# Kernel optimization log

Hardware: AMD Instinct MI355X
Metric: run time of the kernel (lower is better)

The kernel has to match this reference:

```python
import jax, jax.numpy as jnp
import numpy as np

B, N, C = 8, 4096, 768
H, HD = 12, 64          # num_heads, head_dim = C // H
M = HD * 2              # rand_feat_dim
LAM = 0.3
NUM_STEP = 5


def setup_inputs() -> dict:
    key = jax.random.key(0)
    k1, k2, k3, k4 = jax.random.split(key, 4)
    x = jax.random.normal(k1, (B, N, C), dtype=jnp.float32)
    Wqkv = jax.random.normal(k2, (C, 2 * C), dtype=jnp.float32) * 0.02
    Wproj = jax.random.normal(k3, (C, C), dtype=jnp.float32) * 0.02
    bproj = jnp.zeros((C,), dtype=jnp.float32)
    rand_matrix = jax.random.normal(k4, (H, HD, M), dtype=jnp.float32)
    return {"x": x, "Wqkv": Wqkv, "Wproj": Wproj, "bproj": bproj,
            "rand_matrix": rand_matrix}


def _soft(z, t):
    # sign(z) * relu(|z| - t): soft-thresholding (ISTA proximal step)
    return jnp.sign(z) * jax.nn.relu(jnp.abs(z) - t)


def reference(x, Wqkv, Wproj, bproj, rand_matrix):
    Bn, Nn, Cn = x.shape
    Hh, hd, m = rand_matrix.shape
    scale = hd ** (-0.5)

    qkv = x @ Wqkv                                   # [B,N,2C]
    q = qkv[..., :Cn].reshape(Bn, Nn, Hh, hd).transpose(0, 2, 1, 3)  # [B,H,N,hd]
    v = qkv[..., Cn:].reshape(Bn, Nn, Hh, hd).transpose(0, 2, 1, 3)  # [B,H,N,hd]

    # random-feature map: exp(q @ proj - ||q||^2 / 2) / sqrt(m)
    qs = q * scale ** 0.5
    rf = jnp.exp(jnp.einsum('bhnd,hdm->bhnm', qs, rand_matrix)
                 - 0.5 * jnp.sum(qs * qs, axis=-1, keepdims=True)) / m ** 0.5
    # F.normalize(p=2, dim=-2): normalize over the sequence axis
    qn = rf / jnp.maximum(jnp.linalg.norm(rf, axis=-2, keepdims=True), 1e-12)

    kk = jnp.einsum('bhnm,bhnp->bhmp', qn, qn)       # [B,H,m,m]
    kv = jnp.einsum('bhnm,bhnd->bhmd', qn, v)        # [B,H,m,hd]

    # Lipschitz bound: max row L1 norm of kk, detached
    L = jax.lax.stop_gradient(
        jnp.max(jnp.sum(jnp.abs(kk), axis=-1), axis=-1))[..., None, None] + 1.0

    # unrolled ISTA soft-thresholding loop
    s = _soft(kv, LAM)
    for _ in range(NUM_STEP):
        s = _soft(s - (kk @ s - kv) / L, LAM / L)

    out = jnp.einsum('bhnm,bhmd->bhnd', qn, s)       # [B,H,N,hd]
    out = out.transpose(0, 2, 1, 3).reshape(Bn, Nn, Cn)
    return out @ Wproj + bproj
```

## Files before the change

### kernel.cpp

```cpp
#include <hip/hip_runtime.h>


typedef __attribute__((ext_vector_type(8))) short bf16x8;
typedef __attribute__((ext_vector_type(4))) float f32x4;

#define GLD16(gptr, lptr)                                                              \
  __builtin_amdgcn_global_load_lds((const __attribute__((address_space(1))) void*)(gptr), \
                                   (__attribute__((address_space(3))) void*)(lptr), 16, 0, 0)

__device__ __forceinline__ unsigned short f2bf(float f) {
  union { float f; unsigned int u; } v; v.f = f;
  unsigned int r = v.u + 0x7fffu + ((v.u >> 16) & 1u);
  return (unsigned short)(r >> 16);
}
__device__ __forceinline__ float bf2f(unsigned short s) {
  union { unsigned int u; float f; } v; v.u = ((unsigned int)s) << 16;
  return v.f;
}
__device__ __forceinline__ float rn_of(float css) {
  return 1.f / fmaxf(sqrtf(css), 1e-12f);
}

template<int ITERS>
__device__ __forceinline__ void gemm256_core(
    const unsigned short* __restrict__ A,
    const unsigned short* __restrict__ B,
    int ldk,
    f32x4 (&acc)[8][4],
    unsigned short* smem) {
  const int tid = threadIdx.x;
  const int lane = tid & 63, wave = tid >> 6;
  const int l16 = lane & 15, quad = lane >> 4;
  const int wr = wave >> 2, wc = wave & 3;
  const int rsw = l16 & 7;

#pragma unroll
  for (int i = 0; i < 8; i++)
#pragma unroll
    for (int j = 0; j < 4; j++)
#pragma unroll
      for (int r = 0; r < 4; r++) acc[i][j][r] = 0.f;

  const int srow0 = tid >> 3, sc0 = ((tid & 7) ^ (srow0 & 7)) << 3;
  const int srow1 = (tid + 512) >> 3, sc1 = ((tid & 7) ^ (srow1 & 7)) << 3;
  const int dstw = wave * 512;

  auto stageA = [&](int T, int h) {
    const unsigned short* g = A + (long)(h * 128) * ldk + T * 64;
    unsigned short* d = smem + (T & 1) * 32768 + h * 8192 + dstw;
    GLD16(g + (long)srow0 * ldk + sc0, d);
    GLD16(g + (long)srow1 * ldk + sc1, d + 4096);
  };
  auto stageB = [&](int T, int h) {
    const unsigned short* g = B + (long)(h * 128) * ldk + T * 64;
    unsigned short* d = smem + (T & 1) * 32768 + 16384 + h * 8192 + dstw;
    GLD16(g + (long)srow0 * ldk + sc0, d);
    GLD16(g + (long)srow1 * ldk + sc1, d + 4096);
  };

  bf16x8 af[4][2], bn[4][2];

  auto rdA_ks = [&](int b, int mh, int ks) {
    const unsigned short* p = smem + b * 32768 + wr * 8192 + (mh * 64 + l16) * 64;
#pragma unroll
    for (int ii = 0; ii < 4; ii++)
      af[ii][ks] = *(const bf16x8*)(p + ii * 1024 + (((ks * 4 + quad) ^ rsw) << 3));
  };
  auto rdB_ks = [&](int b, int ks) {
    const unsigned short* p = smem + b * 32768 + 16384 + (wc >> 1) * 8192 +
                              ((wc & 1) * 64 + l16) * 64;
#pragma unroll
    for (int jj = 0; jj < 4; jj++)
      bn[jj][ks] = *(const bf16x8*)(p + jj * 1024 + (((ks * 4 + quad) ^ rsw) << 3));
  };

  auto mma16 = [&](int mh, int ks) {
    __builtin_amdgcn_s_setprio(1);
#pragma unroll
    for (int ii = 0; ii < 4; ii++)
#pragma unroll
      for (int jj = 0; jj < 4; jj++)
        acc[mh * 4 + ii][jj] = __builtin_amdgcn_mfma_f32_16x16x32_bf16(
            af[ii][ks], bn[jj][ks], acc[mh * 4 + ii][jj], 0, 0, 0);
    __builtin_amdgcn_s_setprio(0);
  };

#define FENCE asm volatile("" ::: "memory")
#define SGB __builtin_amdgcn_sched_barrier(0)
#define LGKM(n) asm volatile("s_waitcnt lgkmcnt(" #n ")" ::: "memory")

  stageA(0, 0); stageA(0, 1); stageB(0, 0); stageB(0, 1);
  stageB(1, 0); stageB(1, 1);
  asm volatile("s_waitcnt vmcnt(4)" ::: "memory");
  __builtin_amdgcn_s_barrier();

#pragma unroll 1
  for (int i = 0; i < ITERS; i++) {
    const int u = 2 * i;
    const bool more = (i + 1 < ITERS);
    stageA(u + 1, 0);
    rdB_ks(0, 0); rdA_ks(0, 0, 0);
    SGB;
    rdB_ks(0, 1); rdA_ks(0, 0, 1);
    FENCE; __builtin_amdgcn_s_barrier();
    LGKM(8); SGB;
    mma16(0, 0);
    LGKM(0); SGB;
    mma16(0, 1);
    FENCE; __builtin_amdgcn_s_barrier();
    stageA(u + 1, 1);
    if (more) stageB(u + 2, 0);
    rdA_ks(0, 1, 0);
    SGB;
    rdA_ks(0, 1, 1);
    FENCE; __builtin_amdgcn_s_barrier();
    LGKM(4); SGB;
    mma16(1, 0);
    LGKM(0); SGB;
    mma16(1, 1);
    if (more) { asm volatile("s_waitcnt vmcnt(2)" ::: "memory"); }
    else      { asm volatile("s_waitcnt vmcnt(0)" ::: "memory"); }
    FENCE; __builtin_amdgcn_s_barrier();
    if (more) { stageB(u + 2, 1); stageA(u + 2, 0); stageA(u + 2, 1); }
    rdB_ks(1, 0); rdA_ks(1, 0, 0);
    SGB;
    rdB_ks(1, 1); rdA_ks(1, 0, 1);
    FENCE; __builtin_amdgcn_s_barrier();
    LGKM(8); SGB;
    mma16(0, 0);
    LGKM(0); SGB;
    mma16(0, 1);
    FENCE; __builtin_amdgcn_s_barrier();
    if (more) { stageB(u + 3, 0); stageB(u + 3, 1); }
    rdA_ks(1, 1, 0);
    SGB;
    rdA_ks(1, 1, 1);
    FENCE; __builtin_amdgcn_s_barrier();
    LGKM(4); SGB;
    mma16(1, 0);
    LGKM(0); SGB;
    mma16(1, 1);
    if (more) { asm volatile("s_waitcnt vmcnt(4)" ::: "memory"); }
    FENCE; __builtin_amdgcn_s_barrier();
  }
#undef FENCE
#undef SGB
#undef LGKM
}

__global__ __launch_bounds__(256) void k_convert_bf16(const float* __restrict__ in,
                                                      unsigned short* __restrict__ out, long n4) {
  long i = (long)blockIdx.x * 256 + threadIdx.x;
  if (i < n4) {
    float4 v = ((const float4*)in)[i];
    unsigned short o[4] = {f2bf(v.x), f2bf(v.y), f2bf(v.z), f2bf(v.w)};
    ((uint2*)out)[i] = *(uint2*)o;
  }
}

__global__ __launch_bounds__(256) void k_transpose_tiled(const float* __restrict__ in,
                                                         unsigned short* __restrict__ out,
                                                         int R, int C, float scale) {
  __shared__ float t[32][33];
  const float* ib = in + (long)blockIdx.z * R * C;
  unsigned short* ob = out + (long)blockIdx.z * R * C;
  int c0 = blockIdx.x * 32, r0 = blockIdx.y * 32;
  int tx = threadIdx.x & 31, ty = threadIdx.x >> 5;
#pragma unroll
  for (int k = 0; k < 32; k += 8)
    t[ty + k][tx] = ib[(long)(r0 + ty + k) * C + c0 + tx];
  __syncthreads();
#pragma unroll
  for (int k = 0; k < 32; k += 8)
    ob[(long)(c0 + ty + k) * R + r0 + tx] = f2bf(t[tx][ty + k] * scale);
}

__global__ __launch_bounds__(512, 2) void k_gemm_qkv256(const unsigned short* __restrict__ xbf,
                                                        const unsigned short* __restrict__ wqkvT,
                                                        unsigned short* __restrict__ q,
                                                        unsigned short* __restrict__ vT) {
  __shared__ __align__(16) unsigned short smem[65536];
  f32x4 acc[8][4];
  const int L = blockIdx.x;
  const int xcd = L & 7, slot = L >> 3;
  const int rt = xcd * 16 + slot / 6;
  const int ct = slot % 6;
  gemm256_core<6>(xbf + (long)rt * 256 * 768, wqkvT + (long)ct * 256 * 768, 768, acc, smem);

  const int tid = threadIdx.x, lane = tid & 63, wave = tid >> 6;
  const int l16 = lane & 15, quad = lane >> 4;
  const int wr = wave >> 2, wc = wave & 3;
  const int b = rt >> 4;
  const int nbase = (rt & 15) * 256;
  if (ct < 3) {
    unsigned short* pool = smem;
    for (int hh = 0; hh < 2; hh++) {
      __syncthreads();
      if (wr == hh) {
#pragma unroll
        for (int i = 0; i < 8; i++)
#pragma unroll
          for (int j = 0; j < 4; j++)
#pragma unroll
            for (int r = 0; r < 4; r++)
              pool[(i * 16 + quad * 4 + r) * 268 + wc * 64 + j * 16 + l16] = f2bf(acc[i][j][r]);
      }
      __syncthreads();
#pragma unroll
      for (int it = 0; it < 8; it++) {
        int cc = it * 512 + tid;
        int row = cc >> 5, c8 = cc & 31;
        uint4 val = *(const uint4*)&pool[row * 268 + c8 * 8];
        int h = ct * 4 + (c8 >> 3), d = (c8 & 7) * 8;
        long n = nbase + hh * 128 + row;
        *(uint4*)&q[((long)(b * 12 + h) * 4096 + n) * 64 + d] = val;
      }
    }
  } else {
    unsigned short* pool = smem;
    for (int hh = 0; hh < 2; hh++) {
      __syncthreads();
      if (wr == hh) {
#pragma unroll
        for (int i = 0; i < 8; i++)
#pragma unroll
          for (int j = 0; j < 4; j++)
#pragma unroll
            for (int r = 0; r < 4; r++)
              pool[(wc * 64 + j * 16 + l16) * 136 + i * 16 + quad * 4 + r] = f2bf(acc[i][j][r]);
      }
      __syncthreads();
#pragma unroll
      for (int it = 0; it < 8; it++) {
        int chunk = it * 512 + tid;
        int col = chunk >> 4, ng = chunk & 15;
        uint4 val = *(const uint4*)&pool[col * 136 + ng * 8];
        int vcol = (ct - 3) * 256 + col;
        int h = vcol >> 6, d = vcol & 63;
        long n = nbase + hh * 128 + ng * 8;
        *(uint4*)&vT[((long)(b * 12 + h) * 64 + d) * 4096 + n] = val;
      }
    }
  }
}

__global__ __launch_bounds__(256) void k_gemm_rf(const unsigned short* __restrict__ q,
                                                 const unsigned short* __restrict__ rmT,
                                                 unsigned short* __restrict__ qnT,
                                                 float* __restrict__ colss) {
  __shared__ __align__(16) unsigned short smem[16384];
  __shared__ float hnp[256];
  __shared__ float css[128];
  unsigned short* Asm = smem;
  unsigned short* Bsm = smem + 8192;
  unsigned short* pool = smem;
  f32x4 acc[4][4];
  const int nt = blockIdx.x, bh = blockIdx.y, h = bh % 12;
  const int tid = threadIdx.x, lane = tid & 63, wave = tid >> 6;
  const int l16 = lane & 15, quad = lane >> 4;
  const int wm = (wave >> 1) * 64, wn = (wave & 1) * 64;
  const int fsw = (l16 >> 1) & 3;
  const unsigned short* Aq = q + ((long)bh * 4096 + nt * 128) * 64;
  const unsigned short* Brm = rmT + (long)h * 8192;

#pragma unroll
  for (int c = 0; c < 4; c++) {
    int chunk = c * 256 + tid;
    int row = chunk >> 3, ko8 = chunk & 7;
    int kc = ko8 >> 2;
    int c2s = (ko8 & 3) ^ ((row >> 1) & 3);
    *(uint4*)(Asm + kc * 4096 + row * 32 + c2s * 8) = *(const uint4*)(Aq + (long)row * 64 + ko8 * 8);
    *(uint4*)(Bsm + kc * 4096 + row * 32 + c2s * 8) = *(const uint4*)(Brm + (long)row * 64 + ko8 * 8);
  }
  for (int i = tid; i < 128; i += 256) css[i] = 0.f;
  __syncthreads();
  {
    const unsigned short* ap = Asm + (tid & 1) * 4096 + (tid >> 1) * 32;
    float ssum = 0.f;
#pragma unroll
    for (int e = 0; e < 32; e++) { float f = bf2f(ap[e]); ssum += f * f; }
    hnp[tid] = ssum;
  }
#pragma unroll
  for (int i = 0; i < 4; i++)
#pragma unroll
    for (int j = 0; j < 4; j++)
#pragma unroll
      for (int r = 0; r < 4; r++) acc[i][j][r] = 0.f;
#pragma unroll
  for (int kc = 0; kc < 2; kc++) {
    bf16x8 af[4], bfr[4];
#pragma unroll
    for (int i = 0; i < 4; i++)
      af[i] = *(const bf16x8*)(Asm + kc * 4096 + (wm + i * 16 + l16) * 32 + ((quad ^ fsw) * 8));
#pragma unroll
    for (int j = 0; j < 4; j++)
      bfr[j] = *(const bf16x8*)(Bsm + kc * 4096 + (wn + j * 16 + l16) * 32 + ((quad ^ fsw) * 8));
#pragma unroll
    for (int i = 0; i < 4; i++)
#pragma unroll
      for (int j = 0; j < 4; j++)
        acc[i][j] = __builtin_amdgcn_mfma_f32_16x16x32_bf16(af[i], bfr[j], acc[i][j], 0, 0, 0);
  }
  __syncthreads();
  float hnv[4][4];
#pragma unroll
  for (int i = 0; i < 4; i++)
#pragma unroll
    for (int r = 0; r < 4; r++) {
      int row = wm + i * 16 + quad * 4 + r;
      hnv[i][r] = 0.0625f * (hnp[2 * row] + hnp[2 * row + 1]);
    }
#pragma unroll
  for (int j = 0; j < 4; j++) {
    int col = wn + j * 16 + l16;
    float cp = 0.f;
#pragma unroll
    for (int i = 0; i < 4; i++)
#pragma unroll
      for (int r = 0; r < 4; r++) {
        float v = __expf(acc[i][j][r] - hnv[i][r]) * 0.08838834764831845f;
        acc[i][j][r] = v;
        cp += v * v;
      }
    atomicAdd(&css[col], cp);
  }
  __syncthreads();
  for (int i = tid; i < 128; i += 256) atomicAdd(&colss[bh * 128 + i], css[i]);
  for (int hh = 0; hh < 2; hh++) {
    __syncthreads();
    if ((wave >> 1) == hh) {
#pragma unroll
      for (int i = 0; i < 4; i++)
#pragma unroll
        for (int j = 0; j < 4; j++)
#pragma unroll
          for (int r = 0; r < 4; r++)
            pool[(i * 16 + quad * 4 + r) * 134 + wn + j * 16 + l16] = f2bf(acc[i][j][r]);
    }
    __syncthreads();
#pragma unroll
    for (int c = 0; c < 4; c++) {
      int chunk = tid + c * 256;
      int m = chunk >> 3, nj = (chunk & 7) * 8;
      unsigned short o[8];
#pragma unroll
      for (int e = 0; e < 8; e++) o[e] = pool[(nj + e) * 134 + m];
      *(uint4*)&qnT[((long)bh * 128 + m) * 4096 + nt * 128 + hh * 64 + nj] = *(uint4*)o;
    }
  }
}

__global__ __launch_bounds__(256) void k_gemm_kkkv(const unsigned short* __restrict__ qnT,
                                                   const unsigned short* __restrict__ vT,
                                                   const float* __restrict__ colss,
                                                   unsigned short* __restrict__ kkp) {
  __shared__ __align__(16) unsigned short As[128 * 32], Bs[64 * 32];
  f32x4 acc[4][6];
  const int ks = blockIdx.x, bh = blockIdx.y;
  const unsigned short* A = qnT + (long)bh * 128 * 4096 + ks * 512;
  const unsigned short* B1 = vT + (long)bh * 64 * 4096 + ks * 512;
  const int tid = threadIdx.x, lane = tid & 63, wave = tid >> 6;
  const int l16 = lane & 15, quad = lane >> 4;
  const int wm = (wave >> 1) * 64, wn = (wave & 1) * 96;
  const int arow = tid >> 2;
  const int akos = (((tid & 3) ^ ((arow >> 1) & 3)) << 3);
  const int fsw = (l16 >> 1) & 3;
#pragma unroll
  for (int i = 0; i < 4; i++)
#pragma unroll
    for (int j = 0; j < 6; j++)
#pragma unroll
      for (int r = 0; r < 4; r++) acc[i][j][r] = 0.f;
  for (int k0 = 0; k0 < 512; k0 += 32) {
    __syncthreads();
    GLD16(A + (long)arow * 4096 + k0 + akos, As + wave * 512);
    GLD16(A + (long)(arow + 64) * 4096 + k0 + akos, As + 2048 + wave * 512);
    GLD16(B1 + (long)arow * 4096 + k0 + akos, Bs + wave * 512);
    __syncthreads();
    bf16x8 af[4], bfr[6];
#pragma unroll
    for (int i = 0; i < 4; i++)
      af[i] = *(const bf16x8*)(As + (wm + i * 16 + l16) * 32 + ((quad ^ fsw) * 8));
#pragma unroll
    for (int j = 0; j < 6; j++) {
      int row = wn + j * 16 + l16;
      const unsigned short* rp = (row < 128) ? (As + row * 32) : (Bs + (row - 128) * 32);
      bfr[j] = *(const bf16x8*)(rp + ((quad ^ fsw) * 8));
    }
#pragma unroll
    for (int i = 0; i < 4; i++)
#pragma unroll
      for (int j = 0; j < 6; j++)
        acc[i][j] = __builtin_amdgcn_mfma_f32_16x16x32_bf16(af[i], bfr[j], acc[i][j], 0, 0, 0);
  }
  unsigned short* dst = kkp + ((long)ks * 96 + bh) * 24576;
  float rnr[4][4];
#pragma unroll
  for (int i = 0; i < 4; i++)
#pragma unroll
    for (int r = 0; r < 4; r++)
      rnr[i][r] = rn_of(colss[bh * 128 + wm + i * 16 + quad * 4 + r]);
#pragma unroll
  for (int j = 0; j < 6; j++) {
    int col = wn + j * 16 + l16;
    float rnc = (col < 128) ? rn_of(colss[bh * 128 + col]) : 1.f;
#pragma unroll
    for (int i = 0; i < 4; i++)
#pragma unroll
      for (int r = 0; r < 4; r++) {
        int row = wm + i * 16 + quad * 4 + r;
        dst[row * 192 + col] = f2bf(acc[i][j][r] * rnr[i][r] * rnc);
      }
  }
}

__global__ __launch_bounds__(256) void k_ista(const unsigned short* __restrict__ kkp,
                                              const float* __restrict__ colss,
                                              unsigned short* __restrict__ sT) {
  __shared__ __align__(16) unsigned short kks[128 * 144];
  __shared__ __align__(16) unsigned short ssT[64 * 144];
  __shared__ float kvs[128 * 64];
  __shared__ float red[128];
  __shared__ float rns[128];
  const int tid = threadIdx.x, lane = tid & 63, wave = tid >> 6;
  const int l16 = lane & 15, quad = lane >> 4;
  const int wm = (wave >> 1) * 64, wn = (wave & 1) * 32;
  const int bh = blockIdx.x;
  const unsigned short* base = kkp + (long)bh * 24576;
  for (int idx = tid; idx < 3072; idx += 256) {
    int m = idx / 24, c8 = idx % 24;
    float f[8] = {0.f, 0.f, 0.f, 0.f, 0.f, 0.f, 0.f, 0.f};
#pragma unroll
    for (int ks = 0; ks < 8; ks++) {
      union { uint4 u; unsigned short s[8]; } u;
      u.u = *(const uint4*)(base + (long)ks * 2359296 + m * 192 + c8 * 8);
#pragma unroll
      for (int e = 0; e < 8; e++) f[e] += bf2f(u.s[e]);
    }
    if (c8 < 16) {
#pragma unroll
      for (int e = 0; e < 8; e++) kks[m * 144 + c8 * 8 + e] = f2bf(f[e]);
    } else {
#pragma unroll
      for (int e = 0; e < 8; e++) kvs[m * 64 + (c8 - 16) * 8 + e] = f[e];
    }
  }
  __syncthreads();
  float kv[4][2][4];
#pragma unroll
  for (int i = 0; i < 4; i++)
#pragma unroll
    for (int j = 0; j < 2; j++)
#pragma unroll
      for (int r = 0; r < 4; r++) {
        int m = wm + i * 16 + quad * 4 + r, d = wn + j * 16 + l16;
        kv[i][j][r] = kvs[m * 64 + d];
      }
  if (tid < 128) {
    float rs = 0.f;
    const unsigned short* rp = kks + tid * 144;
    for (int p = 0; p < 128; p++) rs += fabsf(bf2f(rp[p]));
    red[tid] = rs;
    rns[tid] = rn_of(colss[bh * 128 + tid]);
  }
  __syncthreads();
  for (int o = 64; o > 0; o >>= 1) {
    if (tid < o) red[tid] = fmaxf(red[tid], red[tid + o]);
    __syncthreads();
  }
  const float L = red[0] + 1.f;
  const float invL = 1.f / L;
  const float lamL = 0.3f * invL;
  float sreg[4][2][4];
#pragma unroll
  for (int i = 0; i < 4; i++)
#pragma unroll
    for (int j = 0; j < 2; j++)
#pragma unroll
      for (int r = 0; r < 4; r++) {
        float z = kv[i][j][r];
        float az = fabsf(z) - 0.3f;
        float s = az > 0.f ? copysignf(az, z) : 0.f;
        sreg[i][j][r] = s;
        ssT[(wn + j * 16 + l16) * 144 + wm + i * 16 + quad * 4 + r] = f2bf(s);
      }
  for (int step = 0; step < 5; step++) {
    __syncthreads();
    f32x4 acc[4][2];
#pragma unroll
    for (int i = 0; i < 4; i++)
#pragma unroll
      for (int j = 0; j < 2; j++)
#pragma unroll
        for (int r = 0; r < 4; r++) acc[i][j][r] = 0.f;
#pragma unroll
    for (int kc = 0; kc < 4; kc++) {
      bf16x8 af[4], bfj[2];
#pragma unroll
      for (int i = 0; i < 4; i++)
        af[i] = *(const bf16x8*)(kks + (wm + i * 16 + l16) * 144 + kc * 32 + quad * 8);
#pragma unroll
      for (int j = 0; j < 2; j++)
        bfj[j] = *(const bf16x8*)(ssT + (wn + j * 16 + l16) * 144 + kc * 32 + quad * 8);
#pragma unroll
      for (int i = 0; i < 4; i++)
#pragma unroll
        for (int j = 0; j < 2; j++)
          acc[i][j] = __builtin_amdgcn_mfma_f32_16x16x32_bf16(af[i], bfj[j], acc[i][j], 0, 0, 0);
    }
    __syncthreads();
#pragma unroll
    for (int i = 0; i < 4; i++)
#pragma unroll
      for (int j = 0; j < 2; j++)
#pragma unroll
        for (int r = 0; r < 4; r++) {
          float z = sreg[i][j][r] - (acc[i][j][r] - kv[i][j][r]) * invL;
          float az = fabsf(z) - lamL;
          float s = az > 0.f ? copysignf(az, z) : 0.f;
          sreg[i][j][r] = s;
          ssT[(wn + j * 16 + l16) * 144 + wm + i * 16 + quad * 4 + r] = f2bf(s);
        }
  }
#pragma unroll
  for (int i = 0; i < 4; i++)
#pragma unroll
    for (int j = 0; j < 2; j++)
#pragma unroll
      for (int r = 0; r < 4; r++) {
        int m = wm + i * 16 + quad * 4 + r, d = wn + j * 16 + l16;
        sT[(long)bh * 8192 + d * 128 + m] = f2bf(sreg[i][j][r] * rns[m]);
      }
}

__global__ __launch_bounds__(256) void k_gemm_attn(const unsigned short* __restrict__ qnT,
                                                   const unsigned short* __restrict__ sT,
                                                   unsigned short* __restrict__ attn) {
  __shared__ __align__(16) unsigned short As2[4352];
  __shared__ __align__(16) unsigned short Bs[64 * 32];
  f32x4 acc[4][2];
  const int nt = blockIdx.x, bh = blockIdx.y;
  const int b = bh / 12, h = bh % 12;
  const int tid = threadIdx.x, lane = tid & 63, wave = tid >> 6;
  const int l16 = lane & 15, quad = lane >> 4;
  const int wm = (wave >> 1) * 64, wn = (wave & 1) * 32;
  const int fsw = (l16 >> 1) & 3;
#pragma unroll
  for (int i = 0; i < 4; i++)
#pragma unroll
    for (int j = 0; j < 2; j++)
#pragma unroll
      for (int r = 0; r < 4; r++) acc[i][j][r] = 0.f;
  for (int k0 = 0; k0 < 128; k0 += 32) {
    __syncthreads();
#pragma unroll
    for (int it = 0; it < 3; it++) {
      if (it < 2 || tid < 32) {
        int c = it * 256 + tid;
        int p = (c * 241) >> 12;
        int nh = c - p * 17;
        int k = ((p & 7) << 2) + (p >> 3);
        int n8 = (nh < 16 ? nh : 15) << 3;
        const unsigned short* gp = qnT + ((long)bh * 128 + k0 + k) * 4096 + nt * 128 + n8;
        GLD16(gp, As2 + (it * 256 + wave * 64) * 8);
      }
    }
    {
      int dd = tid >> 2;
      int ko = (((tid & 3) ^ ((dd >> 1) & 3)) * 8);
      const unsigned short* gp = sT + ((long)bh * 64 + dd) * 128 + k0 + ko;
      GLD16(gp, Bs + wave * 512);
    }
    __syncthreads();
    bf16x8 af[4], bfr[2];
#pragma unroll
    for (int i = 0; i < 4; i++) {
      union { bf16x8 v; unsigned short s[8]; } u;
#pragma unroll
      for (int e = 0; e < 8; e++) {
        int p = ((e & 3) << 3) + (quad << 1) + (e >> 2);
        u.s[e] = As2[p * 136 + wm + i * 16 + l16];
      }
      af[i] = u.v;
    }
#pragma unroll
    for (int j = 0; j < 2; j++)
      bfr[j] = *(const bf16x8*)&Bs[(wn + j * 16 + l16) * 32 + ((quad ^ fsw) * 8)];
#pragma unroll
    for (int i = 0; i < 4; i++)
#pragma unroll
      for (int j = 0; j < 2; j++)
        acc[i][j] = __builtin_amdgcn_mfma_f32_16x16x32_bf16(af[i], bfr[j], acc[i][j], 0, 0, 0);
  }
#pragma unroll
  for (int i = 0; i < 4; i++)
#pragma unroll
    for (int j = 0; j < 2; j++)
#pragma unroll
      for (int r = 0; r < 4; r++) {
        int n = nt * 128 + wm + i * 16 + quad * 4 + r;
        int dd = wn + j * 16 + l16;
        attn[((long)b * 4096 + n) * 768 + h * 64 + dd] = f2bf(acc[i][j][r]);
      }
}

__global__ __launch_bounds__(512, 2) void k_gemm_proj256(const unsigned short* __restrict__ attn,
                                                         const unsigned short* __restrict__ wprojT,
                                                         const float* __restrict__ bias,
                                                         float* __restrict__ out) {
  __shared__ __align__(16) unsigned short smem[65536];
  f32x4 acc[8][4];
  const int L = blockIdx.x;
  const int xcd = L & 7, slot = L >> 3;
  const int rt = xcd * 16 + slot / 3;
  const int ct = slot % 3;
  gemm256_core<6>(attn + (long)rt * 256 * 768, wprojT + (long)ct * 256 * 768, 768, acc, smem);
  const int tid = threadIdx.x, lane = tid & 63, wave = tid >> 6;
  const int l16 = lane & 15, quad = lane >> 4;
  const int wr = wave >> 2, wc = wave & 3;
  const long row0 = (long)rt * 256 + wr * 128;
#pragma unroll
  for (int i = 0; i < 8; i++)
#pragma unroll
    for (int j = 0; j < 4; j++) {
      int col = ct * 256 + wc * 64 + j * 16 + l16;
      float bv = bias[col];
#pragma unroll
      for (int r = 0; r < 4; r++) {
        long row = row0 + i * 16 + quad * 4 + r;
        out[row * 768 + col] = acc[i][j][r] + bv;
      }
    }
}

extern "C" void kernel_launch(void* const* d_in, const int* in_sizes, int n_in,
                              void* d_out, int out_size, void* d_ws, size_t ws_size,
                              hipStream_t stream) {
  const float* x = (const float*)d_in[0];
  const float* Wqkv = (const float*)d_in[1];
  const float* Wproj = (const float*)d_in[2];
  const float* bproj = (const float*)d_in[3];
  const float* rm = (const float*)d_in[4];
  float* out = (float*)d_out;

  size_t o = 0;
  char* wsb = (char*)d_ws;
  auto take = [&](size_t b) { char* p = wsb + o; o += b; return p; };
  unsigned short* wqkvT = (unsigned short*)take(2359296);
  unsigned short* wprojT = (unsigned short*)take(1179648);
  unsigned short* rmT = (unsigned short*)take(196608);
  unsigned short* q = (unsigned short*)take(50331648);
  unsigned short* vT = (unsigned short*)take(50331648);
  float* colss = (float*)take(49152);
  unsigned short* sT = (unsigned short*)take(1572864);
  if (ws_size < o) return;

  unsigned short* xbf = (unsigned short*)d_out;
  unsigned short* qnT = (unsigned short*)d_out;
  unsigned short* kkp = q;
  unsigned short* attnbf = q;

  hipMemsetAsync(colss, 0, 49152, stream);

  k_convert_bf16<<<24576, 256, 0, stream>>>(x, xbf, 6291456L);
  k_transpose_tiled<<<dim3(48, 24, 1), 256, 0, stream>>>(Wqkv, wqkvT, 768, 1536, 1.0f);
  k_transpose_tiled<<<dim3(24, 24, 1), 256, 0, stream>>>(Wproj, wprojT, 768, 768, 1.0f);
  k_transpose_tiled<<<dim3(4, 2, 12), 256, 0, stream>>>(rm, rmT, 64, 128, 0.3535533905932738f);
  k_gemm_qkv256<<<768, 512, 0, stream>>>(xbf, wqkvT, q, vT);
  k_gemm_rf<<<dim3(32, 96), 256, 0, stream>>>(q, rmT, qnT, colss);
  k_gemm_kkkv<<<dim3(8, 96), 256, 0, stream>>>(qnT, vT, colss, kkp);
  k_ista<<<96, 256, 0, stream>>>(kkp, colss, sT);
  k_gemm_attn<<<dim3(32, 96), 256, 0, stream>>>(qnT, sT, attnbf);
  k_gemm_proj256<<<384, 512, 0, stream>>>(attnbf, wprojT, bproj, out);
}
```

Baseline: 457.5 us.

## Restructure GEMM main loop to one K-tile per iteration with register double buffering

The shared 256x256 GEMM core now processes one 64-wide K tile per loop iteration and stages full A and B tiles two ahead. LDS fragment reads are ping-ponged between two register sets so reads for the next MFMA group overlap the current one, with two barriers per tile instead of four per tile. The Q epilogue also drops its LDS transpose staging and writes bf16 values straight from the accumulators with scalar stores. This removes barrier and staging overhead but risks less-coalesced 2-byte global writes for Q and a full vmcnt(0) wait mid-tile.

```diff
diff --git a/kernel.cpp b/kernel.cpp
--- a/kernel.cpp
+++ b/kernel.cpp
@@ -21,7 +21,7 @@
   return 1.f / fmaxf(sqrtf(css), 1e-12f);
 }
 
-template<int ITERS>
+template<int NT>
 __device__ __forceinline__ void gemm256_core(
     const unsigned short* __restrict__ A,
     const unsigned short* __restrict__ B,
@@ -45,107 +45,86 @@
   const int srow1 = (tid + 512) >> 3, sc1 = ((tid & 7) ^ (srow1 & 7)) << 3;
   const int dstw = wave * 512;
 
-  auto stageA = [&](int T, int h) {
-    const unsigned short* g = A + (long)(h * 128) * ldk + T * 64;
-    unsigned short* d = smem + (T & 1) * 32768 + h * 8192 + dstw;
-    GLD16(g + (long)srow0 * ldk + sc0, d);
-    GLD16(g + (long)srow1 * ldk + sc1, d + 4096);
+  auto stage = [&](int T) {
+    unsigned short* d0 = smem + (T & 1) * 32768;
+#pragma unroll
+    for (int h = 0; h < 2; h++) {
+      const unsigned short* gA = A + (long)(h * 128) * ldk + T * 64;
+      const unsigned short* gB = B + (long)(h * 128) * ldk + T * 64;
+      GLD16(gA + (long)srow0 * ldk + sc0, d0 + h * 8192 + dstw);
+      GLD16(gA + (long)srow1 * ldk + sc1, d0 + h * 8192 + 4096 + dstw);
+      GLD16(gB + (long)srow0 * ldk + sc0, d0 + 16384 + h * 8192 + dstw);
+      GLD16(gB + (long)srow1 * ldk + sc1, d0 + 16384 + h * 8192 + 4096 + dstw);
+    }
   };
-  auto stageB = [&](int T, int h) {
-    const unsigned short* g = B + (long)(h * 128) * ldk + T * 64;
-    unsigned short* d = smem + (T & 1) * 32768 + 16384 + h * 8192 + dstw;
-    GLD16(g + (long)srow0 * ldk + sc0, d);
-    GLD16(g + (long)srow1 * ldk + sc1, d + 4096);
+
+  bf16x8 afA[4], afB[4], bnA[4], bnB[4];
+
+  auto rdA = [&](bf16x8 (&d)[4], int b, int mh, int ks) {
+    const unsigned short* p = smem + b * 32768 + wr * 8192 + (mh * 64 + l16) * 64;
+#pragma unroll
+    for (int ii = 0; ii < 4; ii++)
+      d[ii] = *(const bf16x8*)(p + ii * 1024 + (((ks * 4 + quad) ^ rsw) << 3));
   };
-
-  bf16x8 af[4][2], bn[4][2];
-
-  auto rdA_ks = [&](int b, int mh, int ks) {
-    const unsigned short* p = smem + b * 32768 + wr * 8192 + (mh * 64 + l16) * 64;
-#pragma unroll
-    for (int ii = 0; ii < 4; ii++)
-      af[ii][ks] = *(const bf16x8*)(p + ii * 1024 + (((ks * 4 + quad) ^ rsw) << 3));
-  };
-  auto rdB_ks = [&](int b, int ks) {
+  auto rdB = [&](bf16x8 (&d)[4], int b, int ks) {
     const unsigned short* p = smem + b * 32768 + 16384 + (wc >> 1) * 8192 +
                               ((wc & 1) * 64 + l16) * 64;
 #pragma unroll
     for (int jj = 0; jj < 4; jj++)
-      bn[jj][ks] = *(const bf16x8*)(p + jj * 1024 + (((ks * 4 + quad) ^ rsw) << 3));
+      d[jj] = *(const bf16x8*)(p + jj * 1024 + (((ks * 4 + quad) ^ rsw) << 3));
   };
 
-  auto mma16 = [&](int mh, int ks) {
+  auto mma = [&](int mh, bf16x8 (&a)[4], bf16x8 (&bn)[4]) {
     __builtin_amdgcn_s_setprio(1);
 #pragma unroll
     for (int ii = 0; ii < 4; ii++)
 #pragma unroll
       for (int jj = 0; jj < 4; jj++)
         acc[mh * 4 + ii][jj] = __builtin_amdgcn_mfma_f32_16x16x32_bf16(
-            af[ii][ks], bn[jj][ks], acc[mh * 4 + ii][jj], 0, 0, 0);
+            a[ii], bn[jj], acc[mh * 4 + ii][jj], 0, 0, 0);
     __builtin_amdgcn_s_setprio(0);
   };
 
 #define FENCE asm volatile("" ::: "memory")
 #define SGB __builtin_amdgcn_sched_barrier(0)
 #define LGKM(n) asm volatile("s_waitcnt lgkmcnt(" #n ")" ::: "memory")
-
-  stageA(0, 0); stageA(0, 1); stageB(0, 0); stageB(0, 1);
-  stageB(1, 0); stageB(1, 1);
-  asm volatile("s_waitcnt vmcnt(4)" ::: "memory");
+#define VMC0 asm volatile("s_waitcnt vmcnt(0)" ::: "memory")
+
+  stage(0); stage(1);
+  asm volatile("s_waitcnt vmcnt(8)" ::: "memory");
   __builtin_amdgcn_s_barrier();
+  rdA(afA, 0, 0, 0); rdB(bnA, 0, 0);
+  FENCE;
 
 #pragma unroll 1
-  for (int i = 0; i < ITERS; i++) {
-    const int u = 2 * i;
-    const bool more = (i + 1 < ITERS);
-    stageA(u + 1, 0);
-    rdB_ks(0, 0); rdA_ks(0, 0, 0);
+  for (int t = 0; t < NT; t++) {
+    const int b = t & 1;
+    const bool last = (t == NT - 1);
+    rdA(afB, b, 1, 0);
+    LGKM(4); SGB;
+    mma(0, afA, bnA);
+    rdA(afA, b, 0, 1); rdB(bnB, b, 1);
+    LGKM(8); SGB;
+    mma(1, afB, bnA);
+    VMC0; FENCE;
+    __builtin_amdgcn_s_barrier();
+    FENCE;
+    rdA(afB, b, 1, 1);
+    LGKM(4); SGB;
+    mma(0, afA, bnB);
+    if (!last) { rdA(afA, b ^ 1, 0, 0); rdB(bnA, b ^ 1, 0); LGKM(8); }
+    else       { LGKM(0); }
     SGB;
-    rdB_ks(0, 1); rdA_ks(0, 0, 1);
-    FENCE; __builtin_amdgcn_s_barrier();
-    LGKM(8); SGB;
-    mma16(0, 0);
-    LGKM(0); SGB;
-    mma16(0, 1);
-    FENCE; __builtin_amdgcn_s_barrier();
-    stageA(u + 1, 1);
-    if (more) stageB(u + 2, 0);
-    rdA_ks(0, 1, 0);
-    SGB;
-    rdA_ks(0, 1, 1);
-    FENCE; __builtin_amdgcn_s_barrier();
-    LGKM(4); SGB;
-    mma16(1, 0);
-    LGKM(0); SGB;
-    mma16(1, 1);
-    if (more) { asm volatile("s_waitcnt vmcnt(2)" ::: "memory"); }
-    else      { asm volatile("s_waitcnt vmcnt(0)" ::: "memory"); }
-    FENCE; __builtin_amdgcn_s_barrier();
-    if (more) { stageB(u + 2, 1); stageA(u + 2, 0); stageA(u + 2, 1); }
-    rdB_ks(1, 0); rdA_ks(1, 0, 0);
-    SGB;
-    rdB_ks(1, 1); rdA_ks(1, 0, 1);
-    FENCE; __builtin_amdgcn_s_barrier();
-    LGKM(8); SGB;
-    mma16(0, 0);
-    LGKM(0); SGB;
-    mma16(0, 1);
-    FENCE; __builtin_amdgcn_s_barrier();
-    if (more) { stageB(u + 3, 0); stageB(u + 3, 1); }
-    rdA_ks(1, 1, 0);
-    SGB;
-    rdA_ks(1, 1, 1);
-    FENCE; __builtin_amdgcn_s_barrier();
-    LGKM(4); SGB;
-    mma16(1, 0);
-    LGKM(0); SGB;
-    mma16(1, 1);
-    if (more) { asm volatile("s_waitcnt vmcnt(4)" ::: "memory"); }
-    FENCE; __builtin_amdgcn_s_barrier();
+    mma(1, afB, bnB);
+    FENCE;
+    __builtin_amdgcn_s_barrier();
+    FENCE;
+    if (t + 2 < NT) stage(t + 2);
   }
 #undef FENCE
 #undef SGB
 #undef LGKM
+#undef VMC0
 }
 
 __global__ __launch_bounds__(256) void k_convert_bf16(const float* __restrict__ in,
@@ -185,7 +164,7 @@
   const int xcd = L & 7, slot = L >> 3;
   const int rt = xcd * 16 + slot / 6;
   const int ct = slot % 6;
-  gemm256_core<6>(xbf + (long)rt * 256 * 768, wqkvT + (long)ct * 256 * 768, 768, acc, smem);
+  gemm256_core<12>(xbf + (long)rt * 256 * 768, wqkvT + (long)ct * 256 * 768, 768, acc, smem);
 
   const int tid = threadIdx.x, lane = tid & 63, wave = tid >> 6;
   const int l16 = lane & 15, quad = lane >> 4;
@@ -193,29 +172,18 @@
   const int b = rt >> 4;
   const int nbase = (rt & 15) * 256;
   if (ct < 3) {
-    unsigned short* pool = smem;
-    for (int hh = 0; hh < 2; hh++) {
-      __syncthreads();
-      if (wr == hh) {
-#pragma unroll
-        for (int i = 0; i < 8; i++)
-#pragma unroll
-          for (int j = 0; j < 4; j++)
-#pragma unroll
-            for (int r = 0; r < 4; r++)
-              pool[(i * 16 + quad * 4 + r) * 268 + wc * 64 + j * 16 + l16] = f2bf(acc[i][j][r]);
-      }
-      __syncthreads();
-#pragma unroll
-      for (int it = 0; it < 8; it++) {
-        int cc = it * 512 + tid;
-        int row = cc >> 5, c8 = cc & 31;
-        uint4 val = *(const uint4*)&pool[row * 268 + c8 * 8];
-        int h = ct * 4 + (c8 >> 3), d = (c8 & 7) * 8;
-        long n = nbase + hh * 128 + row;
-        *(uint4*)&q[((long)(b * 12 + h) * 4096 + n) * 64 + d] = val;
-      }
-    }
+#pragma unroll
+    for (int i = 0; i < 8; i++)
+#pragma unroll
+      for (int j = 0; j < 4; j++) {
+        int col = ct * 256 + wc * 64 + j * 16 + l16;
+        int h = col >> 6, d = col & 63;
+#pragma unroll
+        for (int r = 0; r < 4; r++) {
+          int n = nbase + wr * 128 + i * 16 + quad * 4 + r;
+          q[((long)(b * 12 + h) * 4096 + n) * 64 + d] = f2bf(acc[i][j][r]);
+        }
+      }
   } else {
     unsigned short* pool = smem;
     for (int hh = 0; hh < 2; hh++) {
@@ -615,7 +583,7 @@
   const int xcd = L & 7, slot = L >> 3;
   const int rt = xcd * 16 + slot / 3;
   const int ct = slot % 3;
-  gemm256_core<6>(attn + (long)rt * 256 * 768, wprojT + (long)ct * 256 * 768, 768, acc, smem);
+  gemm256_core<12>(attn + (long)rt * 256 * 768, wprojT + (long)ct * 256 * 768, 768, acc, smem);
   const int tid = threadIdx.x, lane = tid & 63, wave = tid >> 6;
   const int l16 = lane & 15, quad = lane >> 4;
   const int wr = wave >> 2, wc = wave & 3;
```

New measurement: 455.4 us. Within noise of the previous version (-0.5%).
